# Optimization experiments

Measured on AMD Instinct MI355X. Metric: run time of the kernel, lower is better.

Reference implementation:

```python
import jax, jax.numpy as jnp
import numpy as np

Q, S, D = 8192, 30, 512
THRESH = 30


def setup_inputs() -> dict:
    key = jax.random.key(0)
    ks = jax.random.split(key, 8)
    return {
        "query_encode": jax.random.normal(ks[0], (Q, D), jnp.float32),
        "support_encode": jax.random.normal(ks[1], (S, D), jnp.float32),
        # binary CTR-style labels in {0,1}
        "support_y": jnp.round(jax.random.uniform(ks[2], (1, S), jnp.float32)),
        "support_predict": jax.random.normal(ks[3], (S,), jnp.float32),
        "query_predict": jax.random.normal(ks[4], (Q,), jnp.float32),
        "fc1_w": jax.random.normal(ks[5], (D,), jnp.float32) / np.sqrt(D),
        "fc1_b": jnp.zeros((), jnp.float32),
        # AdjustLayer params: scale init 6, bias init 0, shape [THRESH, 1]
        "adjust_scale": jnp.full((THRESH, 1), 6.0, jnp.float32),
        "adjust_bias": jnp.zeros((THRESH, 1), jnp.float32),
        "num_samples": S,
    }


def reference(query_encode, support_encode, support_y, support_predict,
              query_predict, fc1_w, fc1_b, adjust_scale, adjust_bias,
              num_samples):
    # Pairwise L1 distance: [Q, S, D]
    distance = jnp.abs(query_encode[:, None, :] - support_encode[None, :, :])
    # Linear scorer over feature dim -> [Q, S]
    similar_score = jnp.einsum("qsd,d->qs", distance, fc1_w) + fc1_b
    attn = jax.nn.softmax(similar_score, axis=1)  # softmax over support dim
    # Residual of support labels vs predictor output: [1, S]
    delta_y = support_y - jax.nn.sigmoid(support_predict)[None, :]
    delta_y_hat = jnp.sum(delta_y * attn, axis=1)  # [Q]
    # AdjustLayer: indexed scale/bias (index is a static int here)
    scale = jnp.abs(adjust_scale[num_samples - 1, 0])
    bias = adjust_bias[num_samples - 1, 0]
    prediction = delta_y_hat * scale + bias + query_predict  # [Q]
    # Mean L2 distance to support set: [Q]
    mean_l2 = jnp.mean(jnp.sqrt(jnp.sum(distance ** 2, axis=-1)), axis=-1)
    return prediction, mean_l2
```

## Files before the change

### kernel.cpp

```cpp
#include <hip/hip_runtime.h>
#include <math.h>


#define QN 8192
#define SN 30
#define DN 512
#define BLK 512
#define QT 16
#define SCHUNK 10
#define NPASS 3
#define SROW 580
#define PRW 17
#define PSTR 31

__global__ __launch_bounds__(BLK, 2)
void resus_one(const float* __restrict__ query,
               const float* __restrict__ support,
               const float* __restrict__ support_y,
               const float* __restrict__ support_pr,
               const float* __restrict__ query_pr,
               const float* __restrict__ fc1_w,
               const float* __restrict__ adj_scale,
               const float* __restrict__ adj_bias,
               const int*   __restrict__ num_samples,
               float* __restrict__ out)
{
    __shared__ float  sp[SCHUNK * SROW];
    __shared__ float  praw_sc[SCHUNK * QT * PRW];
    __shared__ float  praw_sq[SCHUNK * QT * PRW];
    __shared__ float2 part[QT * PSTR];

    const int tid   = threadIdx.x;
    const int ql    = tid & 15;
    const int dseg  = (tid >> 4) & 15;
    const int shalf = tid >> 8;
    const int q     = blockIdx.x * QT + ql;

    const float4* sg0 = reinterpret_cast<const float4*>(support);
    float4 g0 = sg0[tid];
    float4 g1 = sg0[tid + 512];
    float4 g2;
    const bool has2 = (tid < 256);
    if (has2) g2 = sg0[tid + 1024];

    const float* qp = query + (size_t)q * DN + dseg * 32;
    const float* wp = fc1_w + dseg * 32;
    float4 a0 = *reinterpret_cast<const float4*>(qp +  0);
    float4 w0 = *reinterpret_cast<const float4*>(wp +  0);
    float4 a1 = *reinterpret_cast<const float4*>(qp +  4);
    float4 w1 = *reinterpret_cast<const float4*>(wp +  4);
    float4 a2 = *reinterpret_cast<const float4*>(qp +  8);
    float4 w2 = *reinterpret_cast<const float4*>(wp +  8);
    float4 a3 = *reinterpret_cast<const float4*>(qp + 12);
    float4 w3 = *reinterpret_cast<const float4*>(wp + 12);
    float4 a4 = *reinterpret_cast<const float4*>(qp + 16);
    float4 w4 = *reinterpret_cast<const float4*>(wp + 16);
    float4 a5 = *reinterpret_cast<const float4*>(qp + 20);
    float4 w5 = *reinterpret_cast<const float4*>(wp + 20);
    float4 a6 = *reinterpret_cast<const float4*>(qp + 24);
    float4 w6 = *reinterpret_cast<const float4*>(wp + 24);
    float4 a7 = *reinterpret_cast<const float4*>(qp + 28);
    float4 w7 = *reinterpret_cast<const float4*>(wp + 28);

    {
        int i = tid, row = i >> 7, c4 = i & 127;
        *reinterpret_cast<float4*>(sp + row * SROW + 36 * (c4 >> 3) + 4 * (c4 & 7)) = g0;
        i = tid + 512; row = i >> 7; c4 = i & 127;
        *reinterpret_cast<float4*>(sp + row * SROW + 36 * (c4 >> 3) + 4 * (c4 & 7)) = g1;
        if (has2) {
            i = tid + 1024; row = i >> 7; c4 = i & 127;
            *reinterpret_cast<float4*>(sp + row * SROW + 36 * (c4 >> 3) + 4 * (c4 & 7)) = g2;
        }
    }
    __syncthreads();

#define ACCD(QV, WV, SV, SC, SQ) { float d_; \
    d_ = (QV).x - (SV).x; SC = fmaf((WV).x, fabsf(d_), SC); SQ = fmaf(d_, d_, SQ); \
    d_ = (QV).y - (SV).y; SC = fmaf((WV).y, fabsf(d_), SC); SQ = fmaf(d_, d_, SQ); \
    d_ = (QV).z - (SV).z; SC = fmaf((WV).z, fabsf(d_), SC); SQ = fmaf(d_, d_, SQ); \
    d_ = (QV).w - (SV).w; SC = fmaf((WV).w, fabsf(d_), SC); SQ = fmaf(d_, d_, SQ); }

    const int sbase = dseg * 36;
    const int pbase = ql * PRW + dseg;
    const int sl0   = shalf * (SCHUNK / 2);

    {
        const float* r0 = sp + (sl0 + 0) * SROW + sbase;
        const float* r1 = sp + (sl0 + 1) * SROW + sbase;
        const float* r2 = sp + (sl0 + 2) * SROW + sbase;
        const float* r3 = sp + (sl0 + 3) * SROW + sbase;
        const float* r4 = sp + (sl0 + 4) * SROW + sbase;
        float sc0 = 0.0f, sc1 = 0.0f, sc2 = 0.0f, sc3 = 0.0f, sc4 = 0.0f;
        float sq0 = 0.0f, sq1 = 0.0f, sq2 = 0.0f, sq3 = 0.0f, sq4 = 0.0f;

#define SEG0(AJ, WJ, OFF) { float4 s_; \
    s_ = *reinterpret_cast<const float4*>(r0 + (OFF)); ACCD(AJ, WJ, s_, sc0, sq0); \
    s_ = *reinterpret_cast<const float4*>(r1 + (OFF)); ACCD(AJ, WJ, s_, sc1, sq1); \
    s_ = *reinterpret_cast<const float4*>(r2 + (OFF)); ACCD(AJ, WJ, s_, sc2, sq2); \
    s_ = *reinterpret_cast<const float4*>(r3 + (OFF)); ACCD(AJ, WJ, s_, sc3, sq3); \
    s_ = *reinterpret_cast<const float4*>(r4 + (OFF)); ACCD(AJ, WJ, s_, sc4, sq4); }

        SEG0(a0, w0,  0) SEG0(a1, w1,  4) SEG0(a2, w2,  8) SEG0(a3, w3, 12)
        SEG0(a4, w4, 16) SEG0(a5, w5, 20) SEG0(a6, w6, 24) SEG0(a7, w7, 28)
#undef SEG0

        praw_sc[(sl0 + 0) * (QT * PRW) + pbase] = sc0;
        praw_sq[(sl0 + 0) * (QT * PRW) + pbase] = sq0;
        praw_sc[(sl0 + 1) * (QT * PRW) + pbase] = sc1;
        praw_sq[(sl0 + 1) * (QT * PRW) + pbase] = sq1;
        praw_sc[(sl0 + 2) * (QT * PRW) + pbase] = sc2;
        praw_sq[(sl0 + 2) * (QT * PRW) + pbase] = sq2;
        praw_sc[(sl0 + 3) * (QT * PRW) + pbase] = sc3;
        praw_sq[(sl0 + 3) * (QT * PRW) + pbase] = sq3;
        praw_sc[(sl0 + 4) * (QT * PRW) + pbase] = sc4;
        praw_sq[(sl0 + 4) * (QT * PRW) + pbase] = sq4;
    }

#define PIN4(V) asm volatile("" : "+v"((V).x), "+v"((V).y), "+v"((V).z), "+v"((V).w))
    PIN4(a0); PIN4(a1); PIN4(a2); PIN4(a3);
    PIN4(a4); PIN4(a5); PIN4(a6); PIN4(a7);
    PIN4(w0); PIN4(w1); PIN4(w2); PIN4(w3);
    PIN4(w4); PIN4(w5); PIN4(w6); PIN4(w7);
#undef PIN4

    __syncthreads();

    if (tid < SCHUNK * QT) {
        const int sl = tid >> 4, qq = tid & 15;
        const int b = sl * (QT * PRW) + qq * PRW;
        float sc = 0.0f, sq = 0.0f;
#pragma unroll
        for (int d = 0; d < 16; ++d) {
            sc += praw_sc[b + d];
            sq += praw_sq[b + d];
        }
        part[qq * PSTR + sl] = make_float2(sc, sq);
    }

#define ACC4(QV, WV, SV) { float d_; \
    d_ = (QV).x - (SV).x; sc = fmaf((WV).x, fabsf(d_), sc); sq = fmaf(d_, d_, sq); \
    d_ = (QV).y - (SV).y; sc = fmaf((WV).y, fabsf(d_), sc); sq = fmaf(d_, d_, sq); \
    d_ = (QV).z - (SV).z; sc = fmaf((WV).z, fabsf(d_), sc); sq = fmaf(d_, d_, sq); \
    d_ = (QV).w - (SV).w; sc = fmaf((WV).w, fabsf(d_), sc); sq = fmaf(d_, d_, sq); }

    for (int pass = 1; pass < NPASS; ++pass) {
        __syncthreads();

        const float4* sg = reinterpret_cast<const float4*>(
            support + (size_t)pass * SCHUNK * DN);
        for (int i = tid; i < SCHUNK * 128; i += BLK) {
            const int row = i >> 7, c4 = i & 127;
            *reinterpret_cast<float4*>(
                sp + row * SROW + 36 * (c4 >> 3) + 4 * (c4 & 7)) = sg[i];
        }
        __syncthreads();

#pragma unroll
        for (int k = 0; k < SCHUNK / 2; ++k) {
            const int sl = sl0 + k;
            const float* sr = sp + sl * SROW + sbase;
            const float4 s0 = *reinterpret_cast<const float4*>(sr +  0);
            const float4 s1 = *reinterpret_cast<const float4*>(sr +  4);
            const float4 s2 = *reinterpret_cast<const float4*>(sr +  8);
            const float4 s3 = *reinterpret_cast<const float4*>(sr + 12);
            const float4 s4 = *reinterpret_cast<const float4*>(sr + 16);
            const float4 s5 = *reinterpret_cast<const float4*>(sr + 20);
            const float4 s6 = *reinterpret_cast<const float4*>(sr + 24);
            const float4 s7 = *reinterpret_cast<const float4*>(sr + 28);

            float sc = 0.0f, sq = 0.0f;
            ACC4(a0, w0, s0) ACC4(a1, w1, s1)
            ACC4(a2, w2, s2) ACC4(a3, w3, s3)
            ACC4(a4, w4, s4) ACC4(a5, w5, s5)
            ACC4(a6, w6, s6) ACC4(a7, w7, s7)

            praw_sc[sl * (QT * PRW) + pbase] = sc;
            praw_sq[sl * (QT * PRW) + pbase] = sq;
        }
        __syncthreads();

        if (tid < SCHUNK * QT) {
            const int sl = tid >> 4, qq = tid & 15;
            const int b = sl * (QT * PRW) + qq * PRW;
            float sc = 0.0f, sq = 0.0f;
#pragma unroll
            for (int d = 0; d < 16; ++d) {
                sc += praw_sc[b + d];
                sq += praw_sq[b + d];
            }
            part[qq * PSTR + pass * SCHUNK + sl] = make_float2(sc, sq);
        }
    }
#undef ACC4
#undef ACCD
    __syncthreads();

    const int grp  = tid >> 5;
    const int s32  = tid & 31;
    const bool valid = (s32 < SN);
    const int  si  = valid ? s32 : 0;

    float dy = 0.0f;
    if (valid)
        dy = support_y[s32] - 1.0f / (1.0f + expf(-support_pr[s32]));

    const int ns = num_samples[0];
    const float ascale = fabsf(adj_scale[ns - 1]);
    const float abias  = adj_bias[ns - 1];

    const int qg = blockIdx.x * QT + grp;
    const float2 pr = part[grp * PSTR + si];

    float scv = valid ? pr.x : -1e30f;
    float ssv = valid ? pr.y : 0.0f;

    float m = scv;
#pragma unroll
    for (int off = 16; off >= 1; off >>= 1)
        m = fmaxf(m, __shfl_xor(m, off));

    float e   = valid ? expf(scv - m) : 0.0f;
    float den = e;
    float num = dy * e;
    float l2  = valid ? sqrtf(ssv) : 0.0f;
#pragma unroll
    for (int off = 16; off >= 1; off >>= 1) {
        den += __shfl_xor(den, off);
        num += __shfl_xor(num, off);
        l2  += __shfl_xor(l2,  off);
    }

    if (s32 == 0) {
        out[qg]      = num / den * ascale + abias + query_pr[qg];
        out[QN + qg] = l2 * (1.0f / (float)SN);
    }
}

extern "C" void kernel_launch(void* const* d_in, const int* in_sizes, int n_in,
                              void* d_out, int out_size, void* d_ws, size_t ws_size,
                              hipStream_t stream)
{
    const float* query      = (const float*)d_in[0];
    const float* support    = (const float*)d_in[1];
    const float* support_y  = (const float*)d_in[2];
    const float* support_pr = (const float*)d_in[3];
    const float* query_pr   = (const float*)d_in[4];
    const float* fc1_w      = (const float*)d_in[5];
    const float* adj_scale  = (const float*)d_in[7];
    const float* adj_bias   = (const float*)d_in[8];
    const int*   num_s      = (const int*)d_in[9];
    float* out = (float*)d_out;

    dim3 grid(QN / QT);
    hipLaunchKernelGGL(resus_one, grid, dim3(BLK), 0, stream,
                       query, support, support_y, support_pr, query_pr,
                       fc1_w, adj_scale, adj_bias, num_s, out);
}
```

Baseline: 94.00 us.

## Prefetch next support chunk into registers while computing current chunk

The pass loop is unrolled and the global loads of each next support chunk are issued into registers before the compute on the current chunk. The chunk is then written into shared memory after the barrier, so global-load latency overlaps the distance computation instead of stalling between passes. The first chunk is now staged before the query and weight loads. This costs extra live registers (12 more floats), which under launch bounds of 2 blocks per SM could raise register pressure or spilling.

New measurement: 98.41 us. 1.05x slower.

```diff
diff --git a/kernel.cpp b/kernel.cpp
--- a/kernel.cpp
+++ b/kernel.cpp
@@ -35,13 +35,23 @@
     const int dseg  = (tid >> 4) & 15;
     const int shalf = tid >> 8;
     const int q     = blockIdx.x * QT + ql;
-
-    const float4* sg0 = reinterpret_cast<const float4*>(support);
-    float4 g0 = sg0[tid];
-    float4 g1 = sg0[tid + 512];
-    float4 g2;
     const bool has2 = (tid < 256);
-    if (has2) g2 = sg0[tid + 1024];
+
+#define SCAT(V, I) { const int i_ = (I), row_ = i_ >> 7, c4_ = i_ & 127; \
+    *reinterpret_cast<float4*>(sp + row_ * SROW + 36 * (c4_ >> 3) + 4 * (c4_ & 7)) = (V); }
+
+    {
+        const float4* sg0 = reinterpret_cast<const float4*>(support);
+        float4 g0 = sg0[tid];
+        float4 g1 = sg0[tid + 512];
+        float4 g2;
+        if (has2) g2 = sg0[tid + 1024];
+        SCAT(g0, tid)
+        SCAT(g1, tid + 512)
+        if (has2) SCAT(g2, tid + 1024)
+    }
+    __syncthreads();
+    asm volatile("" ::: "memory");
 
     const float* qp = query + (size_t)q * DN + dseg * 32;
     const float* wp = fc1_w + dseg * 32;
@@ -62,17 +72,11 @@
     float4 a7 = *reinterpret_cast<const float4*>(qp + 28);
     float4 w7 = *reinterpret_cast<const float4*>(wp + 28);
 
-    {
-        int i = tid, row = i >> 7, c4 = i & 127;
-        *reinterpret_cast<float4*>(sp + row * SROW + 36 * (c4 >> 3) + 4 * (c4 & 7)) = g0;
-        i = tid + 512; row = i >> 7; c4 = i & 127;
-        *reinterpret_cast<float4*>(sp + row * SROW + 36 * (c4 >> 3) + 4 * (c4 & 7)) = g1;
-        if (has2) {
-            i = tid + 1024; row = i >> 7; c4 = i & 127;
-            *reinterpret_cast<float4*>(sp + row * SROW + 36 * (c4 >> 3) + 4 * (c4 & 7)) = g2;
-        }
-    }
-    __syncthreads();
+    const float4* sg1 = reinterpret_cast<const float4*>(support + (size_t)SCHUNK * DN);
+    float4 h0 = sg1[tid];
+    float4 h1 = sg1[tid + 512];
+    float4 h2;
+    if (has2) h2 = sg1[tid + 1024];
 
 #define ACCD(QV, WV, SV, SC, SQ) { float d_; \
     d_ = (QV).x - (SV).x; SC = fmaf((WV).x, fabsf(d_), SC); SQ = fmaf(d_, d_, SQ); \
@@ -125,6 +129,10 @@
 
     __syncthreads();
 
+    SCAT(h0, tid)
+    SCAT(h1, tid + 512)
+    if (has2) SCAT(h2, tid + 1024)
+
     if (tid < SCHUNK * QT) {
         const int sl = tid >> 4, qq = tid & 15;
         const int b = sl * (QT * PRW) + qq * PRW;
@@ -136,6 +144,14 @@
         }
         part[qq * PSTR + sl] = make_float2(sc, sq);
     }
+    __syncthreads();
+    asm volatile("" ::: "memory");
+
+    const float4* sg2 = reinterpret_cast<const float4*>(support + (size_t)2 * SCHUNK * DN);
+    float4 k0 = sg2[tid];
+    float4 k1 = sg2[tid + 512];
+    float4 k2;
+    if (has2) k2 = sg2[tid + 1024];
 
 #define ACC4(QV, WV, SV) { float d_; \
     d_ = (QV).x - (SV).x; sc = fmaf((WV).x, fabsf(d_), sc); sq = fmaf(d_, d_, sq); \
@@ -143,56 +159,66 @@
     d_ = (QV).z - (SV).z; sc = fmaf((WV).z, fabsf(d_), sc); sq = fmaf(d_, d_, sq); \
     d_ = (QV).w - (SV).w; sc = fmaf((WV).w, fabsf(d_), sc); sq = fmaf(d_, d_, sq); }
 
-    for (int pass = 1; pass < NPASS; ++pass) {
-        __syncthreads();
-
-        const float4* sg = reinterpret_cast<const float4*>(
-            support + (size_t)pass * SCHUNK * DN);
-        for (int i = tid; i < SCHUNK * 128; i += BLK) {
-            const int row = i >> 7, c4 = i & 127;
-            *reinterpret_cast<float4*>(
-                sp + row * SROW + 36 * (c4 >> 3) + 4 * (c4 & 7)) = sg[i];
+#define HOTPASS \
+    _Pragma("unroll") \
+    for (int k = 0; k < SCHUNK / 2; ++k) { \
+        const int sl = sl0 + k; \
+        const float* sr = sp + sl * SROW + sbase; \
+        const float4 s0 = *reinterpret_cast<const float4*>(sr +  0); \
+        const float4 s1 = *reinterpret_cast<const float4*>(sr +  4); \
+        const float4 s2 = *reinterpret_cast<const float4*>(sr +  8); \
+        const float4 s3 = *reinterpret_cast<const float4*>(sr + 12); \
+        const float4 s4 = *reinterpret_cast<const float4*>(sr + 16); \
+        const float4 s5 = *reinterpret_cast<const float4*>(sr + 20); \
+        const float4 s6 = *reinterpret_cast<const float4*>(sr + 24); \
+        const float4 s7 = *reinterpret_cast<const float4*>(sr + 28); \
+        float sc = 0.0f, sq = 0.0f; \
+        ACC4(a0, w0, s0) ACC4(a1, w1, s1) \
+        ACC4(a2, w2, s2) ACC4(a3, w3, s3) \
+        ACC4(a4, w4, s4) ACC4(a5, w5, s5) \
+        ACC4(a6, w6, s6) ACC4(a7, w7, s7) \
+        praw_sc[sl * (QT * PRW) + pbase] = sc; \
+        praw_sq[sl * (QT * PRW) + pbase] = sq; \
+    }
+
+    HOTPASS
+    __syncthreads();
+
+    SCAT(k0, tid)
+    SCAT(k1, tid + 512)
+    if (has2) SCAT(k2, tid + 1024)
+
+    if (tid < SCHUNK * QT) {
+        const int sl = tid >> 4, qq = tid & 15;
+        const int b = sl * (QT * PRW) + qq * PRW;
+        float sc = 0.0f, sq = 0.0f;
+#pragma unroll
+        for (int d = 0; d < 16; ++d) {
+            sc += praw_sc[b + d];
+            sq += praw_sq[b + d];
         }
-        __syncthreads();
-
-#pragma unroll
-        for (int k = 0; k < SCHUNK / 2; ++k) {
-            const int sl = sl0 + k;
-            const float* sr = sp + sl * SROW + sbase;
-            const float4 s0 = *reinterpret_cast<const float4*>(sr +  0);
-            const float4 s1 = *reinterpret_cast<const float4*>(sr +  4);
-            const float4 s2 = *reinterpret_cast<const float4*>(sr +  8);
-            const float4 s3 = *reinterpret_cast<const float4*>(sr + 12);
-            const float4 s4 = *reinterpret_cast<const float4*>(sr + 16);
-            const float4 s5 = *reinterpret_cast<const float4*>(sr + 20);
-            const float4 s6 = *reinterpret_cast<const float4*>(sr + 24);
-            const float4 s7 = *reinterpret_cast<const float4*>(sr + 28);
-
-            float sc = 0.0f, sq = 0.0f;
-            ACC4(a0, w0, s0) ACC4(a1, w1, s1)
-            ACC4(a2, w2, s2) ACC4(a3, w3, s3)
-            ACC4(a4, w4, s4) ACC4(a5, w5, s5)
-            ACC4(a6, w6, s6) ACC4(a7, w7, s7)
-
-            praw_sc[sl * (QT * PRW) + pbase] = sc;
-            praw_sq[sl * (QT * PRW) + pbase] = sq;
+        part[qq * PSTR + SCHUNK + sl] = make_float2(sc, sq);
+    }
+    __syncthreads();
+
+    HOTPASS
+    __syncthreads();
+
+    if (tid < SCHUNK * QT) {
+        const int sl = tid >> 4, qq = tid & 15;
+        const int b = sl * (QT * PRW) + qq * PRW;
+        float sc = 0.0f, sq = 0.0f;
+#pragma unroll
+        for (int d = 0; d < 16; ++d) {
+            sc += praw_sc[b + d];
+            sq += praw_sq[b + d];
         }
-        __syncthreads();
-
-        if (tid < SCHUNK * QT) {
-            const int sl = tid >> 4, qq = tid & 15;
-            const int b = sl * (QT * PRW) + qq * PRW;
-            float sc = 0.0f, sq = 0.0f;
-#pragma unroll
-            for (int d = 0; d < 16; ++d) {
-                sc += praw_sc[b + d];
-                sq += praw_sq[b + d];
-            }
-            part[qq * PSTR + pass * SCHUNK + sl] = make_float2(sc, sq);
-        }
-    }
+        part[qq * PSTR + 2 * SCHUNK + sl] = make_float2(sc, sq);
+    }
+#undef HOTPASS
 #undef ACC4
 #undef ACCD
+#undef SCAT
     __syncthreads();
 
     const int grp  = tid >> 5;
```
